# Optimization experiments

Measured on AMD Instinct MI355X. Metric: run time of the kernel, lower is better.

## Reference

```python
import jax, jax.numpy as jnp
import numpy as np

B, N, NPOINT, NSAMPLE = 16, 16384, 512, 32
RADIUS = 0.2
MLP = [64, 64, 128]
CIN = 9  # 3 (xyz) + 6 (point features)
EPS = 1e-5


def setup_inputs() -> dict:
    key = jax.random.key(0)
    ks = jax.random.split(key, 2 + 2 * len(MLP))
    inp = {
        "xyz": jax.random.normal(ks[0], (B, 3, N), dtype=jnp.float32),
        "points": jax.random.normal(ks[1], (B, 6, N), dtype=jnp.float32),
    }
    last = CIN
    for i, oc in enumerate(MLP):
        inp[f"W{i}"] = jax.random.normal(ks[2 + 2 * i], (oc, last), dtype=jnp.float32) / np.sqrt(last)
        inp[f"b{i}"] = jax.random.normal(ks[3 + 2 * i], (oc,), dtype=jnp.float32) * 0.01
        inp[f"g{i}"] = jnp.ones((oc,), jnp.float32)
        inp[f"be{i}"] = jnp.zeros((oc,), jnp.float32)
        last = oc
    return inp


def _fps(xyz):  # xyz: [B,N,3] -> centroid indices [B,NPOINT]
    Bn, Nn, _ = xyz.shape
    init = jnp.zeros((Bn,), jnp.int32)  # torch uses randint; fixed start for determinism

    def step(carry, _):
        dist, far = carry
        cen = jnp.take_along_axis(xyz, far[:, None, None], axis=1)  # [B,1,3]
        d = jnp.sum((xyz - cen) ** 2, axis=-1)                      # [B,N]
        dist = jnp.minimum(dist, d)
        return (dist, jnp.argmax(dist, axis=-1).astype(jnp.int32)), far

    (_, _), cents = jax.lax.scan(
        step, (jnp.full((Bn, Nn), 1e10, xyz.dtype), init), None, length=NPOINT)
    return jnp.transpose(cents)  # [B,NPOINT]


def _sqdist(a, b):  # [B,S,3],[B,N,3] -> [B,S,N]
    return (jnp.sum(a * a, -1)[..., None]
            - 2.0 * jnp.einsum('bsc,bnc->bsn', a, b)
            + jnp.sum(b * b, -1)[:, None, :])


def _gather(pts, idx):  # pts [B,N,C], idx [B,...] -> [B,...,C]
    flat = idx.reshape(idx.shape[0], -1)
    out = jnp.take_along_axis(pts, flat[..., None], axis=1)
    return out.reshape(idx.shape + (pts.shape[-1],))


def _ball_query(xyz, new_xyz):  # -> [B,S,NSAMPLE] indices
    sq = _sqdist(new_xyz, xyz)                                   # [B,S,N]
    cand = jnp.where(sq > RADIUS ** 2, N, jnp.arange(N, dtype=jnp.int32))
    neg_top, _ = jax.lax.top_k(-cand, NSAMPLE)                   # smallest NSAMPLE indices
    idx = -neg_top
    return jnp.where(idx == N, idx[..., :1], idx)                # pad misses with first hit


def _forward(xyz, points, params):
    xyz_t = jnp.transpose(xyz, (0, 2, 1))        # [B,N,3]
    pts_t = jnp.transpose(points, (0, 2, 1))     # [B,N,6]

    fps_idx = _fps(xyz_t)                        # [B,S]
    new_xyz = _gather(xyz_t, fps_idx)            # [B,S,3]
    idx = _ball_query(xyz_t, new_xyz)            # [B,S,K]
    grouped_xyz = _gather(xyz_t, idx) - new_xyz[:, :, None, :]   # [B,S,K,3]
    grouped_pts = _gather(pts_t, idx)                            # [B,S,K,6]
    new_points = jnp.concatenate([grouped_xyz, grouped_pts], axis=-1)  # [B,S,K,9]

    x = jnp.transpose(new_points, (0, 3, 2, 1))  # [B,C,K,S]
    for (W, b, g, be) in params:
        x = jnp.einsum('oc,bcks->boks', W, x) + b[None, :, None, None]
        m = jnp.mean(x, axis=(0, 2, 3), keepdims=True)
        v = jnp.mean((x - m) ** 2, axis=(0, 2, 3), keepdims=True)
        x = (x - m) * jax.lax.rsqrt(v + EPS)
        x = jax.nn.relu(x * g[None, :, None, None] + be[None, :, None, None])
    pooled = jnp.max(x, axis=2)                  # [B,C_out,S]
    return jnp.transpose(new_xyz, (0, 2, 1)), pooled


def reference(xyz, points, W0, b0, g0, be0, W1, b1, g1, be1, W2, b2, g2, be2):
    params = [(W0, b0, g0, be0), (W1, b1, g1, be1), (W2, b2, g2, be2)]
    return _forward(xyz, points, params)
```

## Files before the change

### kernel.cpp

```cpp
#include <hip/hip_runtime.h>
#include <hip/hip_fp16.h>
#include <stddef.h>

#define NPTS 16384
#define NB   16
#define NS   512
#define NK   32
#define CNTF 262144.0f

static constexpr size_t O_NXYZ = 32768;
static constexpr size_t O_IDX  = 131072;
static constexpr size_t O_SC   = 1179648;
static constexpr size_t O_P1   = 1181696;
static constexpr size_t O_P2   = 1705984;
static constexpr size_t O_P3   = 2754560;
static constexpr size_t O_MX   = 4851712;
static constexpr size_t O_Y1   = 13240320;
static constexpr size_t O_Y2   = 80349184;

#define DPP_ROR_FMAX(var, n) { \
    int _r = __builtin_amdgcn_update_dpp(0, __float_as_int(var), 0x120 + (n), 0xF, 0xF, false); \
    var = fmaxf(var, __int_as_float(_r)); }

#define DPP_ROR_UMIN(var, n) { \
    int _r = __builtin_amdgcn_update_dpp(0, (var), 0x120 + (n), 0xF, 0xF, false); \
    var = ((unsigned)_r < (unsigned)(var)) ? _r : (var); }

#define DPP_ROR_LEX(vv, ii, n) { \
    int _rv = __builtin_amdgcn_update_dpp(0, __float_as_int(vv), 0x120 + (n), 0xF, 0xF, false); \
    int _ri = __builtin_amdgcn_update_dpp(0, (ii), 0x120 + (n), 0xF, 0xF, false); \
    float _ov = __int_as_float(_rv); \
    bool _tk = (_ov > (vv)) || (_ov == (vv) && _ri < (ii)); \
    vv = _tk ? _ov : (vv); ii = _tk ? _ri : (ii); }

__global__ __launch_bounds__(1024, 4) void fps_kernel(const float* __restrict__ xyz,
    float* __restrict__ out_nx, float* __restrict__ nxyz_c)
{
    const int b = blockIdx.x;
    const int t = threadIdx.x;
    const int lane = t & 63;
    const int w = t >> 6;
    const float* __restrict__ xb = xyz + (size_t)b * (3 * NPTS);

    __shared__ float sxy[2 * NPTS];
    __shared__ float cand_v[2][16];
    __shared__ int   cand_i[2][16];

    float cx = xb[0], cy = xb[NPTS], cz = xb[2 * NPTS];

#define FPS_DECL(i) float z##i, q##i;
    FPS_DECL(0)  FPS_DECL(1)  FPS_DECL(2)  FPS_DECL(3)
    FPS_DECL(4)  FPS_DECL(5)  FPS_DECL(6)  FPS_DECL(7)
    FPS_DECL(8)  FPS_DECL(9)  FPS_DECL(10) FPS_DECL(11)
    FPS_DECL(12) FPS_DECL(13) FPS_DECL(14) FPS_DECL(15)

#define FPS_INIT(i) { int p = (i) * 1024 + t; \
    float xx = xb[p]; float yy = xb[NPTS + p]; \
    sxy[2 * p] = xx; sxy[2 * p + 1] = yy; \
    z##i = xb[2 * NPTS + p]; q##i = 1e10f; }
    FPS_INIT(0)  FPS_INIT(1)  FPS_INIT(2)  FPS_INIT(3)
    FPS_INIT(4)  FPS_INIT(5)  FPS_INIT(6)  FPS_INIT(7)
    FPS_INIT(8)  FPS_INIT(9)  FPS_INIT(10) FPS_INIT(11)
    FPS_INIT(12) FPS_INIT(13) FPS_INIT(14) FPS_INIT(15)
    __syncthreads();

    for (int it = 0; it < NS; ++it) {
        if (t == 0) {
            out_nx[(b * 3 + 0) * NS + it] = cx;
            out_nx[(b * 3 + 1) * NS + it] = cy;
            out_nx[(b * 3 + 2) * NS + it] = cz;
            float* nc = nxyz_c + ((size_t)(b * NS + it)) * 3;
            nc[0] = cx; nc[1] = cy; nc[2] = cz;
        }
        if (it == NS - 1) break;
        const int par = it & 1;
#define FPS_SLOT(i) { \
        float2 xy = *(const float2*)&sxy[2 * ((i) * 1024 + t)]; \
        float ddx = xy.x - cx, ddy = xy.y - cy, ddz = z##i - cz; \
        float dd = ddx * ddx + ddy * ddy + ddz * ddz; \
        q##i = fminf(q##i, dd); }
        FPS_SLOT(0)  FPS_SLOT(1)  FPS_SLOT(2)  FPS_SLOT(3)
        FPS_SLOT(4)  FPS_SLOT(5)  FPS_SLOT(6)  FPS_SLOT(7)
        FPS_SLOT(8)  FPS_SLOT(9)  FPS_SLOT(10) FPS_SLOT(11)
        FPS_SLOT(12) FPS_SLOT(13) FPS_SLOT(14) FPS_SLOT(15)
        float m = fmaxf(fmaxf(fmaxf(q0,  q1),  fmaxf(q2,  q3)),
                        fmaxf(fmaxf(q4,  q5),  fmaxf(q6,  q7)));
        m = fmaxf(m, fmaxf(fmaxf(fmaxf(q8,  q9),  fmaxf(q10, q11)),
                           fmaxf(fmaxf(q12, q13), fmaxf(q14, q15))));
        DPP_ROR_FMAX(m, 1) DPP_ROR_FMAX(m, 2) DPP_ROR_FMAX(m, 4) DPP_ROR_FMAX(m, 8)
        m = fmaxf(m, __int_as_float(__builtin_amdgcn_ds_swizzle(__float_as_int(m), 0x401F)));
        m = fmaxf(m, __shfl_xor(m, 32));
        int slot = 0x7fffffff;
#define FPS_MATCH(i) slot = (q##i == m) ? (i) : slot;
        FPS_MATCH(15) FPS_MATCH(14) FPS_MATCH(13) FPS_MATCH(12)
        FPS_MATCH(11) FPS_MATCH(10) FPS_MATCH(9)  FPS_MATCH(8)
        FPS_MATCH(7)  FPS_MATCH(6)  FPS_MATCH(5)  FPS_MATCH(4)
        FPS_MATCH(3)  FPS_MATCH(2)  FPS_MATCH(1)  FPS_MATCH(0)
        int gi = (slot == 0x7fffffff) ? 0x7fffffff : ((slot << 10) | t);
        DPP_ROR_UMIN(gi, 1) DPP_ROR_UMIN(gi, 2) DPP_ROR_UMIN(gi, 4) DPP_ROR_UMIN(gi, 8)
        { int r = __builtin_amdgcn_ds_swizzle(gi, 0x401F);
          gi = ((unsigned)r < (unsigned)gi) ? r : gi; }
        { int r = __shfl_xor(gi, 32);
          gi = ((unsigned)r < (unsigned)gi) ? r : gi; }
        if (lane == 0) { cand_v[par][w] = m; cand_i[par][w] = gi; }
        __syncthreads();
        {
            const int j = lane & 15;
            float v = cand_v[par][j];
            int  i0 = cand_i[par][j];
            DPP_ROR_LEX(v, i0, 1) DPP_ROR_LEX(v, i0, 2)
            DPP_ROR_LEX(v, i0, 4) DPP_ROR_LEX(v, i0, 8)
            const float2 cxy = *(const float2*)&sxy[2 * i0];
            cx = cxy.x; cy = cxy.y;
            cz = xb[2 * NPTS + i0];
        }
    }
#undef FPS_DECL
#undef FPS_INIT
#undef FPS_SLOT
#undef FPS_MATCH
}

__global__ __launch_bounds__(256) void ballq_kernel(const float* __restrict__ xyz,
    const float* __restrict__ nxyz_c, int* __restrict__ idx)
{
    const int gw = (blockIdx.x * 256 + threadIdx.x) >> 6;
    const int lane = threadIdx.x & 63;
    const int b = gw >> 9;
    const float* xb = xyz + (size_t)b * (3 * NPTS);
    const float* a = nxyz_c + (size_t)gw * 3;
    const float ax = a[0], ay = a[1], az = a[2];
    const float aa = ax * ax + ay * ay + az * az;
    const unsigned long long lmask = (lane == 63) ? 0x7fffffffffffffffull
                                                  : ((1ull << lane) - 1ull);
    int cnt = 0, first = -1;
    int* op = idx + (size_t)gw * NK;
    for (int base = 0; base < NPTS; base += 64) {
        int p = base + lane;
        float bx = xb[p], by = xb[NPTS + p], bz = xb[2 * NPTS + p];
        float bb = bx * bx + by * by + bz * bz;
        float ab = ax * bx + ay * by + az * bz;
        float sq = (aa - 2.0f * ab) + bb;
        bool hit = !(sq > 0.04f);
        unsigned long long m = __ballot(hit);
        if (m) {
            if (first < 0) first = base + (__ffsll((unsigned long long)m) - 1);
            if (hit) {
                int slot = cnt + __popcll(m & lmask);
                if (slot < NK) op[slot] = p;
            }
            cnt += __popcll(m);
            if (cnt >= NK) break;
        }
    }
    if (cnt < NK && lane >= cnt && lane < NK) op[lane] = first;
}

__global__ __launch_bounds__(256) void conv1_kernel(const float* __restrict__ xyz,
    const float* __restrict__ points, const float* __restrict__ nxyz_c,
    const int* __restrict__ idx, const float* __restrict__ W0, const float* __restrict__ b0,
    float* __restrict__ y1, float* __restrict__ part)
{
    const int lane = threadIdx.x & 63;
    const int w = threadIdx.x >> 6;
    const int wid = blockIdx.x * 4 + w;
    float wr[9];
#pragma unroll
    for (int c = 0; c < 9; ++c) wr[c] = W0[lane * 9 + c];
    const float bias = b0[lane];
    float sum = 0.f, sq = 0.f;
    const int r0 = wid * 64;
    for (int rr = 0; rr < 64; ++rr) {
        int r = r0 + rr;
        int b = r >> 14;
        int s = (r >> 5) & 511;
        int pidx = idx[r];
        const float* xb = xyz + (size_t)b * (3 * NPTS);
        const float* pb = points + (size_t)b * (6 * NPTS);
        const float* nc = nxyz_c + ((size_t)(b * NS + s)) * 3;
        float f0 = xb[pidx] - nc[0];
        float f1 = xb[NPTS + pidx] - nc[1];
        float f2 = xb[2 * NPTS + pidx] - nc[2];
        float f3 = pb[pidx];
        float f4 = pb[NPTS + pidx];
        float f5 = pb[2 * NPTS + pidx];
        float f6 = pb[3 * NPTS + pidx];
        float f7 = pb[4 * NPTS + pidx];
        float f8 = pb[5 * NPTS + pidx];
        float acc = bias;
        acc = fmaf(wr[0], f0, acc); acc = fmaf(wr[1], f1, acc); acc = fmaf(wr[2], f2, acc);
        acc = fmaf(wr[3], f3, acc); acc = fmaf(wr[4], f4, acc); acc = fmaf(wr[5], f5, acc);
        acc = fmaf(wr[6], f6, acc); acc = fmaf(wr[7], f7, acc); acc = fmaf(wr[8], f8, acc);
        y1[(size_t)r * 64 + lane] = acc;
        sum += acc; sq = fmaf(acc, acc, sq);
    }
    __shared__ float sred[4 * 128];
    sred[w * 128 + lane] = sum;
    sred[w * 128 + 64 + lane] = sq;
    __syncthreads();
    if (threadIdx.x < 128) {
        float tot = sred[threadIdx.x] + sred[128 + threadIdx.x]
                  + sred[256 + threadIdx.x] + sred[384 + threadIdx.x];
        part[(size_t)blockIdx.x * 128 + threadIdx.x] = tot;
    }
}

__global__ __launch_bounds__(256) void conv2_kernel(const float* __restrict__ y1,
    const float* __restrict__ W1, const float* __restrict__ b1,
    const float* __restrict__ scales, float* __restrict__ y2, float* __restrict__ part)
{
    __shared__ float aT[64 * 128];
    __shared__ float wT[64 * 64];
    __shared__ float sred[4 * 128];
    __shared__ float ssc[128];
    const int tid = threadIdx.x;
    const int r0 = blockIdx.x * 128;

    if (tid < 128) ssc[tid] = scales[tid];
    {
        const int o = tid & 63;
        const int cseg = (tid >> 6) * 16;
#pragma unroll
        for (int j = 0; j < 4; ++j) {
            const float4 v = *(const float4*)&W1[o * 64 + cseg + j * 4];
            wT[(cseg + j * 4 + 0) * 64 + o] = v.x;
            wT[(cseg + j * 4 + 1) * 64 + o] = v.y;
            wT[(cseg + j * 4 + 2) * 64 + o] = v.z;
            wT[(cseg + j * 4 + 3) * 64 + o] = v.w;
        }
    }
    __syncthreads();
    {
        const int r = tid & 127;
        const int cs = (tid >> 7) * 32;
#pragma unroll
        for (int j = 0; j < 8; ++j) {
            const int c = cs + j * 4;
            const float4 v = *(const float4*)&y1[(size_t)(r0 + r) * 64 + c];
            aT[(c + 0) * 128 + r] = fmaxf(fmaf(ssc[c + 0], v.x, ssc[64 + c + 0]), 0.f);
            aT[(c + 1) * 128 + r] = fmaxf(fmaf(ssc[c + 1], v.y, ssc[64 + c + 1]), 0.f);
            aT[(c + 2) * 128 + r] = fmaxf(fmaf(ssc[c + 2], v.z, ssc[64 + c + 2]), 0.f);
            aT[(c + 3) * 128 + r] = fmaxf(fmaf(ssc[c + 3], v.w, ssc[64 + c + 3]), 0.f);
        }
    }
    __syncthreads();

    const int wv = tid >> 6;
    const int lane = tid & 63;
    const int tr = lane >> 4;
    const int to = lane & 15;
    const int rbase = wv * 32 + tr * 8;
    const int obase = to * 4;

    const float4 bv = *(const float4*)&b1[obase];
    float4 acc[8];
#pragma unroll
    for (int rr = 0; rr < 8; ++rr) acc[rr] = bv;

#pragma unroll 4
    for (int c = 0; c < 64; ++c) {
        const float4 a0 = *(const float4*)&aT[c * 128 + rbase];
        const float4 a1 = *(const float4*)&aT[c * 128 + rbase + 4];
        const float4 wf = *(const float4*)&wT[c * 64 + obase];
        const float ar[8] = {a0.x, a0.y, a0.z, a0.w, a1.x, a1.y, a1.z, a1.w};
#pragma unroll
        for (int rr = 0; rr < 8; ++rr) {
            acc[rr].x = fmaf(ar[rr], wf.x, acc[rr].x);
            acc[rr].y = fmaf(ar[rr], wf.y, acc[rr].y);
            acc[rr].z = fmaf(ar[rr], wf.z, acc[rr].z);
            acc[rr].w = fmaf(ar[rr], wf.w, acc[rr].w);
        }
    }
    float4 s = {0.f, 0.f, 0.f, 0.f}, q = {0.f, 0.f, 0.f, 0.f};
#pragma unroll
    for (int rr = 0; rr < 8; ++rr) {
        *(float4*)&y2[(size_t)(r0 + rbase + rr) * 64 + obase] = acc[rr];
        s.x += acc[rr].x; s.y += acc[rr].y; s.z += acc[rr].z; s.w += acc[rr].w;
        q.x = fmaf(acc[rr].x, acc[rr].x, q.x);
        q.y = fmaf(acc[rr].y, acc[rr].y, q.y);
        q.z = fmaf(acc[rr].z, acc[rr].z, q.z);
        q.w = fmaf(acc[rr].w, acc[rr].w, q.w);
    }
#pragma unroll
    for (int off = 16; off <= 32; off <<= 1) {
        s.x += __shfl_xor(s.x, off); s.y += __shfl_xor(s.y, off);
        s.z += __shfl_xor(s.z, off); s.w += __shfl_xor(s.w, off);
        q.x += __shfl_xor(q.x, off); q.y += __shfl_xor(q.y, off);
        q.z += __shfl_xor(q.z, off); q.w += __shfl_xor(q.w, off);
    }
    if (tr == 0) {
        sred[wv * 128 + obase + 0] = s.x; sred[wv * 128 + obase + 1] = s.y;
        sred[wv * 128 + obase + 2] = s.z; sred[wv * 128 + obase + 3] = s.w;
        sred[wv * 128 + 64 + obase + 0] = q.x; sred[wv * 128 + 64 + obase + 1] = q.y;
        sred[wv * 128 + 64 + obase + 2] = q.z; sred[wv * 128 + 64 + obase + 3] = q.w;
    }
    __syncthreads();
    if (tid < 128) {
        float tot = sred[tid] + sred[128 + tid] + sred[256 + tid] + sred[384 + tid];
        part[(size_t)blockIdx.x * 128 + tid] = tot;
    }
}

__global__ __launch_bounds__(256) void conv3_kernel(const float* __restrict__ y2,
    const float* __restrict__ W2, const float* __restrict__ b2,
    const float* __restrict__ scales, __half2* __restrict__ mxmn, float* __restrict__ part)
{
    __shared__ float aT[64 * 128];
    __shared__ float wT[64 * 128];
    __shared__ float sred[4 * 256];
    __shared__ float ssc[128];
    const int tid = threadIdx.x;
    const int r0 = blockIdx.x * 128;

    if (tid < 128) ssc[tid] = scales[128 + tid];
    {
        const int o = tid & 127;
        const int cs = (tid >> 7) * 32;
#pragma unroll
        for (int j = 0; j < 8; ++j) {
            const float4 v = *(const float4*)&W2[(size_t)o * 64 + cs + j * 4];
            wT[(cs + j * 4 + 0) * 128 + o] = v.x;
            wT[(cs + j * 4 + 1) * 128 + o] = v.y;
            wT[(cs + j * 4 + 2) * 128 + o] = v.z;
            wT[(cs + j * 4 + 3) * 128 + o] = v.w;
        }
    }
    __syncthreads();
    {
        const int r = tid & 127;
        const int cs = (tid >> 7) * 32;
#pragma unroll
        for (int j = 0; j < 8; ++j) {
            const int c = cs + j * 4;
            const float4 v = *(const float4*)&y2[(size_t)(r0 + r) * 64 + c];
            aT[(c + 0) * 128 + r] = fmaxf(fmaf(ssc[c + 0], v.x, ssc[64 + c + 0]), 0.f);
            aT[(c + 1) * 128 + r] = fmaxf(fmaf(ssc[c + 1], v.y, ssc[64 + c + 1]), 0.f);
            aT[(c + 2) * 128 + r] = fmaxf(fmaf(ssc[c + 2], v.z, ssc[64 + c + 2]), 0.f);
            aT[(c + 3) * 128 + r] = fmaxf(fmaf(ssc[c + 3], v.w, ssc[64 + c + 3]), 0.f);
        }
    }
    __syncthreads();

    const int wv = tid >> 6;
    const int lane = tid & 63;
    const int tr = lane >> 4;
    const int to = lane & 15;
    const int rbase = wv * 32 + tr * 8;
    const int ol = to * 4;
    const int oh = 64 + to * 4;

    const float4 bl = *(const float4*)&b2[ol];
    const float4 bh = *(const float4*)&b2[oh];
    float4 accl[8], acch[8];
#pragma unroll
    for (int rr = 0; rr < 8; ++rr) { accl[rr] = bl; acch[rr] = bh; }

#pragma unroll 2
    for (int c = 0; c < 64; ++c) {
        const float4 a0 = *(const float4*)&aT[c * 128 + rbase];
        const float4 a1 = *(const float4*)&aT[c * 128 + rbase + 4];
        const float4 w0 = *(const float4*)&wT[c * 128 + ol];
        const float4 w1 = *(const float4*)&wT[c * 128 + oh];
        const float ar[8] = {a0.x, a0.y, a0.z, a0.w, a1.x, a1.y, a1.z, a1.w};
#pragma unroll
        for (int rr = 0; rr < 8; ++rr) {
            accl[rr].x = fmaf(ar[rr], w0.x, accl[rr].x);
            accl[rr].y = fmaf(ar[rr], w0.y, accl[rr].y);
            accl[rr].z = fmaf(ar[rr], w0.z, accl[rr].z);
            accl[rr].w = fmaf(ar[rr], w0.w, accl[rr].w);
            acch[rr].x = fmaf(ar[rr], w1.x, acch[rr].x);
            acch[rr].y = fmaf(ar[rr], w1.y, acch[rr].y);
            acch[rr].z = fmaf(ar[rr], w1.z, acch[rr].z);
            acch[rr].w = fmaf(ar[rr], w1.w, acch[rr].w);
        }
    }
    float4 sl = {0,0,0,0}, ql = {0,0,0,0}, sh4 = {0,0,0,0}, qh = {0,0,0,0};
    float4 mxl = accl[0], mnl = accl[0], mxh = acch[0], mnh = acch[0];
#pragma unroll
    for (int rr = 0; rr < 8; ++rr) {
        sl.x += accl[rr].x; sl.y += accl[rr].y; sl.z += accl[rr].z; sl.w += accl[rr].w;
        sh4.x += acch[rr].x; sh4.y += acch[rr].y; sh4.z += acch[rr].z; sh4.w += acch[rr].w;
        ql.x = fmaf(accl[rr].x, accl[rr].x, ql.x); ql.y = fmaf(accl[rr].y, accl[rr].y, ql.y);
        ql.z = fmaf(accl[rr].z, accl[rr].z, ql.z); ql.w = fmaf(accl[rr].w, accl[rr].w, ql.w);
        qh.x = fmaf(acch[rr].x, acch[rr].x, qh.x); qh.y = fmaf(acch[rr].y, acch[rr].y, qh.y);
        qh.z = fmaf(acch[rr].z, acch[rr].z, qh.z); qh.w = fmaf(acch[rr].w, acch[rr].w, qh.w);
        mxl.x = fmaxf(mxl.x, accl[rr].x); mnl.x = fminf(mnl.x, accl[rr].x);
        mxl.y = fmaxf(mxl.y, accl[rr].y); mnl.y = fminf(mnl.y, accl[rr].y);
        mxl.z = fmaxf(mxl.z, accl[rr].z); mnl.z = fminf(mnl.z, accl[rr].z);
        mxl.w = fmaxf(mxl.w, accl[rr].w); mnl.w = fminf(mnl.w, accl[rr].w);
        mxh.x = fmaxf(mxh.x, acch[rr].x); mnh.x = fminf(mnh.x, acch[rr].x);
        mxh.y = fmaxf(mxh.y, acch[rr].y); mnh.y = fminf(mnh.y, acch[rr].y);
        mxh.z = fmaxf(mxh.z, acch[rr].z); mnh.z = fminf(mnh.z, acch[rr].z);
        mxh.w = fmaxf(mxh.w, acch[rr].w); mnh.w = fminf(mnh.w, acch[rr].w);
    }
#pragma unroll
    for (int off = 16; off <= 32; off <<= 1) {
        sl.x += __shfl_xor(sl.x, off); sl.y += __shfl_xor(sl.y, off);
        sl.z += __shfl_xor(sl.z, off); sl.w += __shfl_xor(sl.w, off);
        sh4.x += __shfl_xor(sh4.x, off); sh4.y += __shfl_xor(sh4.y, off);
        sh4.z += __shfl_xor(sh4.z, off); sh4.w += __shfl_xor(sh4.w, off);
        ql.x += __shfl_xor(ql.x, off); ql.y += __shfl_xor(ql.y, off);
        ql.z += __shfl_xor(ql.z, off); ql.w += __shfl_xor(ql.w, off);
        qh.x += __shfl_xor(qh.x, off); qh.y += __shfl_xor(qh.y, off);
        qh.z += __shfl_xor(qh.z, off); qh.w += __shfl_xor(qh.w, off);
        mxl.x = fmaxf(mxl.x, __shfl_xor(mxl.x, off)); mnl.x = fminf(mnl.x, __shfl_xor(mnl.x, off));
        mxl.y = fmaxf(mxl.y, __shfl_xor(mxl.y, off)); mnl.y = fminf(mnl.y, __shfl_xor(mnl.y, off));
        mxl.z = fmaxf(mxl.z, __shfl_xor(mxl.z, off)); mnl.z = fminf(mnl.z, __shfl_xor(mnl.z, off));
        mxl.w = fmaxf(mxl.w, __shfl_xor(mxl.w, off)); mnl.w = fminf(mnl.w, __shfl_xor(mnl.w, off));
        mxh.x = fmaxf(mxh.x, __shfl_xor(mxh.x, off)); mnh.x = fminf(mnh.x, __shfl_xor(mnh.x, off));
        mxh.y = fmaxf(mxh.y, __shfl_xor(mxh.y, off)); mnh.y = fminf(mnh.y, __shfl_xor(mnh.y, off));
        mxh.z = fmaxf(mxh.z, __shfl_xor(mxh.z, off)); mnh.z = fminf(mnh.z, __shfl_xor(mnh.z, off));
        mxh.w = fmaxf(mxh.w, __shfl_xor(mxh.w, off)); mnh.w = fminf(mnh.w, __shfl_xor(mnh.w, off));
    }
    if (tr == 0) {
        const int wid = blockIdx.x * 4 + wv;
        __half2* mp = mxmn + (size_t)wid * 128;
        mp[ol + 0] = __floats2half2_rn(mxl.x, mnl.x);
        mp[ol + 1] = __floats2half2_rn(mxl.y, mnl.y);
        mp[ol + 2] = __floats2half2_rn(mxl.z, mnl.z);
        mp[ol + 3] = __floats2half2_rn(mxl.w, mnl.w);
        mp[oh + 0] = __floats2half2_rn(mxh.x, mnh.x);
        mp[oh + 1] = __floats2half2_rn(mxh.y, mnh.y);
        mp[oh + 2] = __floats2half2_rn(mxh.z, mnh.z);
        mp[oh + 3] = __floats2half2_rn(mxh.w, mnh.w);
        sred[wv * 256 + ol + 0] = sl.x; sred[wv * 256 + ol + 1] = sl.y;
        sred[wv * 256 + ol + 2] = sl.z; sred[wv * 256 + ol + 3] = sl.w;
        sred[wv * 256 + oh + 0] = sh4.x; sred[wv * 256 + oh + 1] = sh4.y;
        sred[wv * 256 + oh + 2] = sh4.z; sred[wv * 256 + oh + 3] = sh4.w;
        sred[wv * 256 + 128 + ol + 0] = ql.x; sred[wv * 256 + 128 + ol + 1] = ql.y;
        sred[wv * 256 + 128 + ol + 2] = ql.z; sred[wv * 256 + 128 + ol + 3] = ql.w;
        sred[wv * 256 + 128 + oh + 0] = qh.x; sred[wv * 256 + 128 + oh + 1] = qh.y;
        sred[wv * 256 + 128 + oh + 2] = qh.z; sred[wv * 256 + 128 + oh + 3] = qh.w;
    }
    __syncthreads();
    {
        float tot = sred[tid] + sred[256 + tid] + sred[512 + tid] + sred[768 + tid];
        part[(size_t)blockIdx.x * 256 + tid] = tot;
    }
}

__global__ __launch_bounds__(1024) void stats_kernel(const float* __restrict__ part,
    int nparts, int nch, const float* __restrict__ g, const float* __restrict__ be,
    float* __restrict__ scale, float* __restrict__ shift)
{
    __shared__ float s_s[1024], s_q[1024];
    const int t = threadIdx.x;
    const int groups = 1024 / nch;
    const int gid = t / nch;
    const int o = t % nch;
    const int chunk = nparts / groups;
    float sum = 0.f, sq = 0.f;
    for (int p = gid * chunk; p < (gid + 1) * chunk; ++p) {
        sum += part[(size_t)p * 2 * nch + o];
        sq  += part[(size_t)p * 2 * nch + nch + o];
    }
    s_s[t] = sum; s_q[t] = sq;
    __syncthreads();
    if (t < nch) {
        float S = 0.f, Q = 0.f;
        for (int gi = 0; gi < groups; ++gi) { S += s_s[gi * nch + o]; Q += s_q[gi * nch + o]; }
        float m = S / CNTF;
        float v = Q / CNTF - m * m;
        v = v < 0.f ? 0.f : v;
        float scv = g[o] / sqrtf(v + 1e-5f);
        scale[o] = scv;
        shift[o] = be[o] - m * scv;
    }
}

__global__ __launch_bounds__(256) void final_kernel(const __half2* __restrict__ mxmn,
    const float* __restrict__ scales, float* __restrict__ out)
{
    int tid = blockIdx.x * 256 + threadIdx.x;
    int b = tid >> 16;
    int o = (tid >> 9) & 127;
    int s = tid & 511;
    int row = (b * NS + s) * 128 + o;
    float sc = scales[256 + o], sh = scales[384 + o];
    const __half2 h = mxmn[row];
    float vmx = __low2float(h), vmn = __high2float(h);
    float y = fmaxf(fmaf(sc, vmx, sh), fmaf(sc, vmn, sh));
    out[tid] = fmaxf(y, 0.f);
}

extern "C" void kernel_launch(void* const* d_in, const int* in_sizes, int n_in,
                              void* d_out, int out_size, void* d_ws, size_t ws_size,
                              hipStream_t stream)
{
    (void)in_sizes; (void)n_in; (void)out_size; (void)ws_size;
    const float* xyz    = (const float*)d_in[0];
    const float* points = (const float*)d_in[1];
    const float* W0  = (const float*)d_in[2];
    const float* b0  = (const float*)d_in[3];
    const float* g0  = (const float*)d_in[4];
    const float* be0 = (const float*)d_in[5];
    const float* W1  = (const float*)d_in[6];
    const float* b1  = (const float*)d_in[7];
    const float* g1  = (const float*)d_in[8];
    const float* be1 = (const float*)d_in[9];
    const float* W2  = (const float*)d_in[10];
    const float* b2  = (const float*)d_in[11];
    const float* g2  = (const float*)d_in[12];
    const float* be2 = (const float*)d_in[13];

    char* ws = (char*)d_ws;
    float*   nxyz = (float*)(ws + O_NXYZ);
    int*     idx  = (int*)(ws + O_IDX);
    float*   scl  = (float*)(ws + O_SC);
    float*   p1   = (float*)(ws + O_P1);
    float*   p2   = (float*)(ws + O_P2);
    float*   p3   = (float*)(ws + O_P3);
    __half2* mxmn = (__half2*)(ws + O_MX);
    float*   y1   = (float*)(ws + O_Y1);
    float*   y2   = (float*)(ws + O_Y2);
    float*   out  = (float*)d_out;

    fps_kernel<<<16, 1024, 0, stream>>>(xyz, out, nxyz);
    ballq_kernel<<<2048, 256, 0, stream>>>(xyz, nxyz, idx);
    conv1_kernel<<<1024, 256, 0, stream>>>(xyz, points, nxyz, idx, W0, b0, y1, p1);
    stats_kernel<<<1, 1024, 0, stream>>>(p1, 1024, 64, g0, be0, scl + 0, scl + 64);
    conv2_kernel<<<2048, 256, 0, stream>>>(y1, W1, b1, scl, y2, p2);
    stats_kernel<<<1, 1024, 0, stream>>>(p2, 2048, 64, g1, be1, scl + 128, scl + 192);
    conv3_kernel<<<2048, 256, 0, stream>>>(y2, W2, b2, scl, mxmn, p3);
    stats_kernel<<<1, 1024, 0, stream>>>(p3, 2048, 128, g2, be2, scl + 256, scl + 384);
    final_kernel<<<4096, 256, 0, stream>>>(mxmn, scl, out + 24576);
}
```

Before: 1.274 ms.

## Split FPS per batch across four cooperating blocks with global atomic flag exchange

Farthest point sampling for each batch now runs on four workgroups instead of one. Each group owns a quarter of the points, kept in registers, and the groups agree on each iteration's winner through global atomic flags that pack the distance and an inverted index. This spreads the serial FPS loop over four times as many compute units and cuts per-thread work. The cost is a cross-block spin-wait every iteration, which adds global memory latency, plus a memset launch. The scheme depends on all 64 blocks being co-resident, otherwise it deadlocks.

```diff
diff --git a/kernel.cpp b/kernel.cpp
--- a/kernel.cpp
+++ b/kernel.cpp
@@ -15,6 +15,7 @@
 static constexpr size_t O_P2   = 1705984;
 static constexpr size_t O_P3   = 2754560;
 static constexpr size_t O_MX   = 4851712;
+static constexpr size_t O_FLG  = 9046016;
 static constexpr size_t O_Y1   = 13240320;
 static constexpr size_t O_Y2   = 80349184;
 
@@ -34,69 +35,59 @@
     vv = _tk ? _ov : (vv); ii = _tk ? _ri : (ii); }
 
 __global__ __launch_bounds__(1024, 4) void fps_kernel(const float* __restrict__ xyz,
-    float* __restrict__ out_nx, float* __restrict__ nxyz_c)
-{
-    const int b = blockIdx.x;
-    const int t = threadIdx.x;
+    float* __restrict__ out_nx, float* __restrict__ nxyz_c,
+    unsigned long long* __restrict__ flags)
+{
+    const int bb = blockIdx.x >> 2;
+    const int g  = blockIdx.x & 3;
+    const int t  = threadIdx.x;
     const int lane = t & 63;
-    const int w = t >> 6;
-    const float* __restrict__ xb = xyz + (size_t)b * (3 * NPTS);
+    const int w  = t >> 6;
+    const float* __restrict__ xb = xyz + (size_t)bb * (3 * NPTS);
 
     __shared__ float sxy[2 * NPTS];
     __shared__ float cand_v[2][16];
     __shared__ int   cand_i[2][16];
+    __shared__ unsigned long long s_win[2];
+
+    for (int i = 0; i < 16; ++i) {
+        int p = i * 1024 + t;
+        sxy[2 * p]     = xb[p];
+        sxy[2 * p + 1] = xb[NPTS + p];
+    }
+    float x0, x1, x2, x3, y0, y1, y2, y3, z0, z1, z2, z3, q0, q1, q2, q3;
+#define FPS_INIT(i) { int p = (g << 12) + ((i) << 10) + t; \
+    x##i = xb[p]; y##i = xb[NPTS + p]; z##i = xb[2 * NPTS + p]; q##i = 1e10f; }
+    FPS_INIT(0) FPS_INIT(1) FPS_INIT(2) FPS_INIT(3)
+#undef FPS_INIT
+    __syncthreads();
 
     float cx = xb[0], cy = xb[NPTS], cz = xb[2 * NPTS];
 
-#define FPS_DECL(i) float z##i, q##i;
-    FPS_DECL(0)  FPS_DECL(1)  FPS_DECL(2)  FPS_DECL(3)
-    FPS_DECL(4)  FPS_DECL(5)  FPS_DECL(6)  FPS_DECL(7)
-    FPS_DECL(8)  FPS_DECL(9)  FPS_DECL(10) FPS_DECL(11)
-    FPS_DECL(12) FPS_DECL(13) FPS_DECL(14) FPS_DECL(15)
-
-#define FPS_INIT(i) { int p = (i) * 1024 + t; \
-    float xx = xb[p]; float yy = xb[NPTS + p]; \
-    sxy[2 * p] = xx; sxy[2 * p + 1] = yy; \
-    z##i = xb[2 * NPTS + p]; q##i = 1e10f; }
-    FPS_INIT(0)  FPS_INIT(1)  FPS_INIT(2)  FPS_INIT(3)
-    FPS_INIT(4)  FPS_INIT(5)  FPS_INIT(6)  FPS_INIT(7)
-    FPS_INIT(8)  FPS_INIT(9)  FPS_INIT(10) FPS_INIT(11)
-    FPS_INIT(12) FPS_INIT(13) FPS_INIT(14) FPS_INIT(15)
-    __syncthreads();
-
     for (int it = 0; it < NS; ++it) {
-        if (t == 0) {
-            out_nx[(b * 3 + 0) * NS + it] = cx;
-            out_nx[(b * 3 + 1) * NS + it] = cy;
-            out_nx[(b * 3 + 2) * NS + it] = cz;
-            float* nc = nxyz_c + ((size_t)(b * NS + it)) * 3;
+        if (g == 0 && t == 0) {
+            out_nx[(bb * 3 + 0) * NS + it] = cx;
+            out_nx[(bb * 3 + 1) * NS + it] = cy;
+            out_nx[(bb * 3 + 2) * NS + it] = cz;
+            float* nc = nxyz_c + ((size_t)(bb * NS + it)) * 3;
             nc[0] = cx; nc[1] = cy; nc[2] = cz;
         }
         if (it == NS - 1) break;
         const int par = it & 1;
 #define FPS_SLOT(i) { \
-        float2 xy = *(const float2*)&sxy[2 * ((i) * 1024 + t)]; \
-        float ddx = xy.x - cx, ddy = xy.y - cy, ddz = z##i - cz; \
+        float ddx = x##i - cx, ddy = y##i - cy, ddz = z##i - cz; \
         float dd = ddx * ddx + ddy * ddy + ddz * ddz; \
         q##i = fminf(q##i, dd); }
-        FPS_SLOT(0)  FPS_SLOT(1)  FPS_SLOT(2)  FPS_SLOT(3)
-        FPS_SLOT(4)  FPS_SLOT(5)  FPS_SLOT(6)  FPS_SLOT(7)
-        FPS_SLOT(8)  FPS_SLOT(9)  FPS_SLOT(10) FPS_SLOT(11)
-        FPS_SLOT(12) FPS_SLOT(13) FPS_SLOT(14) FPS_SLOT(15)
-        float m = fmaxf(fmaxf(fmaxf(q0,  q1),  fmaxf(q2,  q3)),
-                        fmaxf(fmaxf(q4,  q5),  fmaxf(q6,  q7)));
-        m = fmaxf(m, fmaxf(fmaxf(fmaxf(q8,  q9),  fmaxf(q10, q11)),
-                           fmaxf(fmaxf(q12, q13), fmaxf(q14, q15))));
+        FPS_SLOT(0) FPS_SLOT(1) FPS_SLOT(2) FPS_SLOT(3)
+#undef FPS_SLOT
+        float m = fmaxf(fmaxf(q0, q1), fmaxf(q2, q3));
         DPP_ROR_FMAX(m, 1) DPP_ROR_FMAX(m, 2) DPP_ROR_FMAX(m, 4) DPP_ROR_FMAX(m, 8)
         m = fmaxf(m, __int_as_float(__builtin_amdgcn_ds_swizzle(__float_as_int(m), 0x401F)));
         m = fmaxf(m, __shfl_xor(m, 32));
         int slot = 0x7fffffff;
-#define FPS_MATCH(i) slot = (q##i == m) ? (i) : slot;
-        FPS_MATCH(15) FPS_MATCH(14) FPS_MATCH(13) FPS_MATCH(12)
-        FPS_MATCH(11) FPS_MATCH(10) FPS_MATCH(9)  FPS_MATCH(8)
-        FPS_MATCH(7)  FPS_MATCH(6)  FPS_MATCH(5)  FPS_MATCH(4)
-        FPS_MATCH(3)  FPS_MATCH(2)  FPS_MATCH(1)  FPS_MATCH(0)
-        int gi = (slot == 0x7fffffff) ? 0x7fffffff : ((slot << 10) | t);
+        slot = (q3 == m) ? 3 : slot; slot = (q2 == m) ? 2 : slot;
+        slot = (q1 == m) ? 1 : slot; slot = (q0 == m) ? 0 : slot;
+        int gi = (slot == 0x7fffffff) ? 0x7fffffff : ((g << 12) | (slot << 10) | t);
         DPP_ROR_UMIN(gi, 1) DPP_ROR_UMIN(gi, 2) DPP_ROR_UMIN(gi, 4) DPP_ROR_UMIN(gi, 8)
         { int r = __builtin_amdgcn_ds_swizzle(gi, 0x401F);
           gi = ((unsigned)r < (unsigned)gi) ? r : gi; }
@@ -110,15 +101,34 @@
             int  i0 = cand_i[par][j];
             DPP_ROR_LEX(v, i0, 1) DPP_ROR_LEX(v, i0, 2)
             DPP_ROR_LEX(v, i0, 4) DPP_ROR_LEX(v, i0, 8)
-            const float2 cxy = *(const float2*)&sxy[2 * i0];
+            if (t == 0) {
+                unsigned long long* f = flags + ((size_t)it << 6) + (bb << 2);
+                unsigned long long pw =
+                    ((unsigned long long)(unsigned)__float_as_int(v) << 32)
+                    | (unsigned)(65535 - i0);
+                __hip_atomic_store(&f[g], pw, __ATOMIC_RELEASE, __HIP_MEMORY_SCOPE_AGENT);
+                unsigned long long a0 = 0, a1 = 0, a2 = 0, a3 = 0;
+                for (;;) {
+                    if (!a0) a0 = __hip_atomic_load(&f[0], __ATOMIC_ACQUIRE, __HIP_MEMORY_SCOPE_AGENT);
+                    if (!a1) a1 = __hip_atomic_load(&f[1], __ATOMIC_ACQUIRE, __HIP_MEMORY_SCOPE_AGENT);
+                    if (!a2) a2 = __hip_atomic_load(&f[2], __ATOMIC_ACQUIRE, __HIP_MEMORY_SCOPE_AGENT);
+                    if (!a3) a3 = __hip_atomic_load(&f[3], __ATOMIC_ACQUIRE, __HIP_MEMORY_SCOPE_AGENT);
+                    if (a0 && a1 && a2 && a3) break;
+                }
+                unsigned long long wn = a0 > a1 ? a0 : a1;
+                unsigned long long wm = a2 > a3 ? a2 : a3;
+                s_win[par] = wn > wm ? wn : wm;
+            }
+        }
+        __syncthreads();
+        {
+            const unsigned long long win = s_win[par];
+            const int gw = 65535 - (int)(win & 0xFFFFull);
+            const float2 cxy = *(const float2*)&sxy[2 * gw];
             cx = cxy.x; cy = cxy.y;
-            cz = xb[2 * NPTS + i0];
-        }
-    }
-#undef FPS_DECL
-#undef FPS_INIT
-#undef FPS_SLOT
-#undef FPS_MATCH
+            cz = xb[2 * NPTS + gw];
+        }
+    }
 }
 
 __global__ __launch_bounds__(256) void ballq_kernel(const float* __restrict__ xyz,
@@ -511,11 +521,13 @@
     float*   p2   = (float*)(ws + O_P2);
     float*   p3   = (float*)(ws + O_P3);
     __half2* mxmn = (__half2*)(ws + O_MX);
+    unsigned long long* flags = (unsigned long long*)(ws + O_FLG);
     float*   y1   = (float*)(ws + O_Y1);
     float*   y2   = (float*)(ws + O_Y2);
     float*   out  = (float*)d_out;
 
-    fps_kernel<<<16, 1024, 0, stream>>>(xyz, out, nxyz);
+    hipMemsetAsync(flags, 0, 511 * 16 * 4 * sizeof(unsigned long long), stream);
+    fps_kernel<<<64, 1024, 0, stream>>>(xyz, out, nxyz, flags);
     ballq_kernel<<<2048, 256, 0, stream>>>(xyz, nxyz, idx);
     conv1_kernel<<<1024, 256, 0, stream>>>(xyz, points, nxyz, idx, W0, b0, y1, p1);
     stats_kernel<<<1, 1024, 0, stream>>>(p1, 1024, 64, g0, be0, scl + 0, scl + 64);
```

Result: slower. 2.004 ms (+57.4%).
